# Kernel optimization log

Measured on AMD Instinct MI355X. Metric: run time of the kernel, lower is better.

## Reference

```python
import jax, jax.numpy as jnp
import numpy as np
from jax import lax

TAU = 0.1
LAMBDA_ABCD = 0.5
NUM_ANCHORS = 256
THRESH = 0.6
NEG_INF = -1e30


def sample_features(feat, anchors):
    # feat: [B,C,H,W], anchors: [B,N,2] in [0,1] (u,v). Bilinear, align_corners=False, zeros padding.
    B, C, H, W = feat.shape
    g = anchors * 2.0 - 1.0
    x = ((g[..., 0] + 1.0) * W - 1.0) / 2.0  # [B,N] pixel coords
    y = ((g[..., 1] + 1.0) * H - 1.0) / 2.0
    x0 = jnp.floor(x).astype(jnp.int32); x1 = x0 + 1
    y0 = jnp.floor(y).astype(jnp.int32); y1 = y0 + 1
    wx1 = x - x0.astype(x.dtype); wx0 = 1.0 - wx1
    wy1 = y - y0.astype(y.dtype); wy0 = 1.0 - wy1
    flat = feat.reshape(B, C, H * W)

    def gather(xi, yi):
        valid = ((xi >= 0) & (xi < W) & (yi >= 0) & (yi < H)).astype(feat.dtype)
        idx = jnp.clip(yi, 0, H - 1) * W + jnp.clip(xi, 0, W - 1)  # [B,N]
        v = jnp.take_along_axis(flat, idx[:, None, :], axis=2)  # [B,C,N]
        return v * valid[:, None, :]

    out = (gather(x0, y0) * (wx0 * wy0)[:, None, :]
           + gather(x1, y0) * (wx1 * wy0)[:, None, :]
           + gather(x0, y1) * (wx0 * wy1)[:, None, :]
           + gather(x1, y1) * (wx1 * wy1)[:, None, :])
    return out.transpose(0, 2, 1)  # [B,N,C]


def layer_norm(x, gamma, beta, eps=1e-5):
    mu = x.mean(-1, keepdims=True)
    var = ((x - mu) ** 2).mean(-1, keepdims=True)
    return (x - mu) * lax.rsqrt(var + eps) * gamma + beta


def l2norm(x, eps=1e-12):
    n = jnp.sqrt(jnp.sum(x * x, -1, keepdims=True))
    return x / jnp.maximum(n, eps)


def conv2d(x, w, b, pad):
    y = lax.conv_general_dilated(x, w, (1, 1), pad,
                                 dimension_numbers=('NCHW', 'OIHW', 'NCHW'))
    return y + b[None, :, None, None]


def setup_inputs() -> dict:
    key = jax.random.key(0)
    ks = jax.random.split(key, 12)
    B, Ct, Cs, H, W, P = 16, 1024, 512, 64, 64, 256
    s = lambda k, shp, fan: jax.random.normal(k, shp, jnp.float32) * (1.0 / np.sqrt(fan))
    return {
        'teacher_feat': jax.random.normal(ks[0], (B, Ct, H, W), jnp.float32),
        'student_feat': jax.random.normal(ks[1], (B, Cs, H, W), jnp.float32),
        'conv1_w': s(ks[2], (Ct // 2, Ct, 3, 3), Ct * 9),
        'conv1_b': jnp.zeros((Ct // 2,), jnp.float32),
        'conv2_w': s(ks[3], (1, Ct // 2, 1, 1), Ct // 2),
        'conv2_b': jnp.zeros((1,), jnp.float32),
        't_w': s(ks[4], (Ct, P), Ct), 't_b': jnp.zeros((P,), jnp.float32),
        't_g': jnp.ones((P,), jnp.float32), 't_beta': jnp.zeros((P,), jnp.float32),
        's_w': s(ks[5], (Cs, P), Cs), 's_b': jnp.zeros((P,), jnp.float32),
        's_g': jnp.ones((P,), jnp.float32), 's_beta': jnp.zeros((P,), jnp.float32),
    }


def reference(teacher_feat, student_feat, conv1_w, conv1_b, conv2_w, conv2_b,
              t_w, t_b, t_g, t_beta, s_w, s_b, s_g, s_beta):
    B, Ct, H, W = teacher_feat.shape
    # learnable anchor generator
    h = jax.nn.relu(conv2d(teacher_feat, conv1_w, conv1_b, 'SAME'))
    heatmap = jax.nn.softplus(conv2d(h, conv2_w, conv2_b, 'SAME'))  # [B,1,H,W]
    prob = heatmap.reshape(B, -1)
    prob = prob / (prob.sum(1, keepdims=True) + 1e-6)
    # multinomial without replacement via Gumbel top-k (fixed key -> deterministic)
    u01 = jax.random.uniform(jax.random.key(42), prob.shape, jnp.float32, 1e-8, 1.0)
    gumbel = -jnp.log(-jnp.log(u01))
    idx = lax.top_k(jnp.log(prob + 1e-12) + gumbel, NUM_ANCHORS)[1]  # [B,N]
    ax = (idx % W).astype(jnp.float32) / W
    ay = (idx // W).astype(jnp.float32) / H
    anchors = jnp.stack([ax, ay], -1)  # [B,N,2]

    ft = sample_features(teacher_feat, anchors)  # [B,N,Ct]
    fs = sample_features(student_feat, anchors)  # [B,N,Cs]
    ft = l2norm(layer_norm(jnp.einsum('bnc,cp->bnp', ft, t_w) + t_b, t_g, t_beta))
    fs = l2norm(layer_norm(jnp.einsum('bnc,cp->bnp', fs, s_w) + s_b, s_g, s_beta))

    loss_gafd = jnp.mean((fs - lax.stop_gradient(ft)) ** 2)

    saliency = sample_features(heatmap, anchors)[..., 0]  # [B,N]
    bd = saliency > THRESH * saliency.max(1, keepdims=True)  # [B,N] bool
    non_bd = ~bd

    pos = jnp.sum(fs * ft, -1) / TAU                       # [B,N]
    neg = jnp.einsum('bnc,bmc->bnm', fs, fs) / TAU          # [B,N,N]
    neg = jnp.where(non_bd[:, None, :], neg, NEG_INF)
    logits = jnp.concatenate([pos[..., None], neg], -1)    # [B,N,N+1]
    row_loss = jax.nn.logsumexp(logits, -1) - pos          # [B,N]

    bd_f = bd.astype(jnp.float32)
    cnt = bd_f.sum(1)
    per_b = (row_loss * bd_f).sum(1) / jnp.maximum(cnt, 1.0)
    valid = ((cnt > 0) & (non_bd.sum(1) > 0)).astype(jnp.float32)
    vnum = valid.sum()
    loss_abcd = jnp.where(vnum > 0, (per_b * valid).sum() / jnp.maximum(vnum, 1.0), 0.0)

    total_loss = loss_gafd + LAMBDA_ABCD * loss_abcd
    return total_loss, loss_gafd, loss_abcd, heatmap
```

## Files before the change

### kernel.cpp

```cpp
#include <hip/hip_runtime.h>
#include <stdint.h>


typedef float f32x4 __attribute__((ext_vector_type(4)));
typedef short s16x8 __attribute__((ext_vector_type(8)));

__device__ __forceinline__ unsigned short f2bf(float f) {
  unsigned u = __float_as_uint(f);
  u += 0x7fffu + ((u >> 16) & 1u);
  return (unsigned short)(u >> 16);
}
__device__ __forceinline__ float bf2f(unsigned short h) {
  return __uint_as_float((unsigned)h << 16);
}

__device__ __forceinline__ void gld16(const void* g, void* l) {
  __builtin_amdgcn_global_load_lds(
      (const __attribute__((address_space(1))) void*)g,
      (__attribute__((address_space(3))) void*)l, 16, 0, 0);
}

__device__ __forceinline__ float block_sum(float v, float* l4) {
  for (int m = 32; m; m >>= 1) v += __shfl_xor(v, m, 64);
  int wid = threadIdx.x >> 6;
  if ((threadIdx.x & 63) == 0) l4[wid] = v;
  __syncthreads();
  float r = l4[0] + l4[1] + l4[2] + l4[3];
  __syncthreads();
  return r;
}

__global__ void k_pad_transpose(const float* __restrict__ teacher,
                                unsigned short* __restrict__ tpad) {
  __shared__ __align__(16) unsigned short lds[64 * 65];
  int bid = blockIdx.x;
  int cb = bid & 15, y = (bid >> 4) & 63, b = bid >> 10;
  int t = threadIdx.x;
#pragma unroll
  for (int it = 0; it < 16; ++it) {
    int idx = it * 256 + t;
    int cl = idx >> 6, x = idx & 63;
    float v = teacher[(size_t)(b * 1024 + cb * 64 + cl) * 4096 + y * 64 + x];
    lds[cl * 65 + x] = f2bf(v);
  }
  __syncthreads();
  size_t obase = ((size_t)(b * 66 + y + 1) * 66 + 1) * 1024 + cb * 64;
#pragma unroll
  for (int it = 0; it < 16; ++it) {
    int x = it * 4 + (t >> 6);
    int cl = t & 63;
    tpad[obase + (size_t)x * 1024 + cl] = lds[cl * 65 + x];
  }
  if (y == 0) {
    for (int idx = t; idx < 66 * 64; idx += 256) {
      int col = idx >> 6, cl = idx & 63;
      tpad[((size_t)(b * 66) * 66 + col) * 1024 + cb * 64 + cl] = 0;
    }
  }
  if (y == 63) {
    for (int idx = t; idx < 66 * 64; idx += 256) {
      int col = idx >> 6, cl = idx & 63;
      tpad[((size_t)(b * 66 + 65) * 66 + col) * 1024 + cb * 64 + cl] = 0;
    }
  }
  if (t < 128) {
    int col = (t >= 64) ? 65 : 0;
    int cl = t & 63;
    tpad[((size_t)(b * 66 + y + 1) * 66 + col) * 1024 + cb * 64 + cl] = 0;
  }
}

__global__ void k_wprep(const float* __restrict__ w1,
                        unsigned short* __restrict__ wt) {
  __shared__ float wl[9216];
  int co = blockIdx.x, t = threadIdx.x;
  const float* src = w1 + (size_t)co * 9216;
  for (int i = t; i < 9216; i += 256) wl[i] = src[i];
  __syncthreads();
  for (int i = t; i < 9216; i += 256) {
    int tap = i >> 10;
    int ci = i - (tap << 10);
    int kb = ci >> 6, kc = ci & 63;
    wt[(size_t)tap * 524288 + (size_t)kb * 32768 + co * 64 + kc] = f2bf(wl[ci * 9 + tap]);
  }
}

__global__ void k_wT(const float* __restrict__ w, unsigned short* __restrict__ wT,
                     int K) {
  int e = blockIdx.x * 256 + threadIdx.x;
  int p = e / K, k = e - p * K;
  wT[e] = f2bf(w[(size_t)k * 256 + p]);
}

__global__ __launch_bounds__(256) void k_conv(
    const unsigned short* __restrict__ tpad, const unsigned short* __restrict__ wt,
    const float* __restrict__ b1, const float* __restrict__ w2,
    float* __restrict__ heat) {
  __shared__ __align__(16) unsigned short As[128 * 64];
  __shared__ __align__(16) unsigned short Bs[128 * 64];
  int bid = blockIdx.x;
  int nt = bid & 3, mt = bid >> 2;
  int p0 = mt * 128;
  int b = p0 >> 12, y0 = (p0 >> 6) & 63;
  int co0 = nt * 128;
  int t = threadIdx.x, wid = t >> 6, lane = t & 63;
  int wm = wid & 1, wn = wid >> 1;
  int quad = lane >> 4, l15 = lane & 15;
  int sw7 = l15 & 7;

  f32x4 acc[4][4];
  const f32x4 fz = {0.f, 0.f, 0.f, 0.f};
#pragma unroll
  for (int i = 0; i < 4; ++i)
#pragma unroll
    for (int j = 0; j < 4; ++j) acc[i][j] = fz;

  int xj[4], yrj[4];
#pragma unroll
  for (int jj = 0; jj < 4; ++jj) {
    int m = (wid * 4 + jj) * 8 + (lane >> 3);
    xj[jj] = m & 63;
    yrj[jj] = m >> 6;
  }
  int kcol = (((lane & 7) ^ ((lane >> 3) & 7))) * 8;
  int brow = ((lane >> 3) & 7) * 64;
  const unsigned short* wt_nt = wt + (size_t)co0 * 64;

  for (int tap = 0; tap < 9; ++tap) {
    int ky = tap / 3, kx = tap - ky * 3;
    size_t abase[4];
#pragma unroll
    for (int jj = 0; jj < 4; ++jj) {
      int row = y0 + yrj[jj] + ky;
      int col = xj[jj] + kx;
      abase[jj] = ((size_t)(b * 66 + row) * 66 + col) * 1024 + kcol;
    }
    size_t bbase = (size_t)tap * 16 * 32768;
    for (int kb = 0; kb < 16; ++kb) {
#pragma unroll
      for (int jj = 0; jj < 4; ++jj) {
        gld16(tpad + abase[jj] + kb * 64, (char*)As + (wid * 4 + jj) * 1024);
        gld16(wt_nt + bbase + (size_t)kb * 32768 + (wid * 4 + jj) * 512 + brow + kcol,
              (char*)Bs + (wid * 4 + jj) * 1024);
      }
      __syncthreads();
#pragma unroll
      for (int s = 0; s < 2; ++s) {
        s16x8 af[4], bf[4];
        int chunk = ((s * 4 + quad) ^ sw7) * 8;
#pragma unroll
        for (int i = 0; i < 4; ++i) {
          af[i] = *(const s16x8*)(const void*)(As + (wm * 64 + i * 16 + l15) * 64 + chunk);
          bf[i] = *(const s16x8*)(const void*)(Bs + (wn * 64 + i * 16 + l15) * 64 + chunk);
        }
#pragma unroll
        for (int i = 0; i < 4; ++i)
#pragma unroll
          for (int j = 0; j < 4; ++j)
            acc[i][j] = __builtin_amdgcn_mfma_f32_16x16x32_bf16(af[i], bf[j], acc[i][j], 0, 0, 0);
      }
      __syncthreads();
    }
  }

  float w2v[4], b1v[4];
#pragma unroll
  for (int j = 0; j < 4; ++j) {
    int co = co0 + wn * 64 + j * 16 + l15;
    w2v[j] = w2[co];
    b1v[j] = b1[co];
  }
#pragma unroll
  for (int i = 0; i < 4; ++i) {
#pragma unroll
    for (int r = 0; r < 4; ++r) {
      float part = 0.f;
#pragma unroll
      for (int j = 0; j < 4; ++j) {
        float v = acc[i][j][r] + b1v[j];
        v = fmaxf(v, 0.f);
        part += v * w2v[j];
      }
#pragma unroll
      for (int msk = 1; msk < 16; msk <<= 1) part += __shfl_xor(part, msk, 64);
      if (l15 == 0) {
        int m = wm * 64 + i * 16 + quad * 4 + r;
        atomicAdd(&heat[p0 + m], part);
      }
    }
  }
}

__device__ __forceinline__ unsigned rotl32(unsigned x, int d) {
  return (x << d) | (x >> (32 - d));
}
__device__ unsigned threefry_bits(unsigned lo) {
  const unsigned k0 = 0u, k1 = 42u;
  const unsigned k2 = 0x1BD11BDAu ^ k0 ^ k1;
  unsigned x0 = 0u + k0, x1 = lo + k1;
#define TF_R4(a, bq, c, d)                                \
  x0 += x1; x1 = rotl32(x1, a); x1 ^= x0;                 \
  x0 += x1; x1 = rotl32(x1, bq); x1 ^= x0;                \
  x0 += x1; x1 = rotl32(x1, c); x1 ^= x0;                 \
  x0 += x1; x1 = rotl32(x1, d); x1 ^= x0;
  TF_R4(13, 15, 26, 6)  x0 += k1; x1 += k2 + 1u;
  TF_R4(17, 29, 16, 24) x0 += k2; x1 += k0 + 2u;
  TF_R4(13, 15, 26, 6)  x0 += k0; x1 += k1 + 3u;
  TF_R4(17, 29, 16, 24) x0 += k1; x1 += k2 + 4u;
  TF_R4(13, 15, 26, 6)  x0 += k2; x1 += k0 + 5u;
#undef TF_R4
  return x0 ^ x1;
}

__global__ void k_heat2score(const float* __restrict__ heat, const float* __restrict__ b2p,
                             float* __restrict__ out_hm, float* __restrict__ hm,
                             float* __restrict__ scores) {
  __shared__ float l4[4];
  int b = blockIdx.x, t = threadIdx.x;
  float b2 = b2p[0];
  float hv[16];
  float lsum = 0.f;
#pragma unroll
  for (int j = 0; j < 16; ++j) {
    int e = j * 256 + t;
    float x = heat[b * 4096 + e] + b2;
    float sp = fmaxf(x, 0.f) + log1pf(expf(-fabsf(x)));
    hv[j] = sp;
    lsum += sp;
  }
  float S = block_sum(lsum, l4);
  float denom = S + 1e-6f;
#pragma unroll
  for (int j = 0; j < 16; ++j) {
    int e = j * 256 + t;
    float sp = hv[j];
    out_hm[b * 4096 + e] = sp;
    hm[b * 4096 + e] = sp;
    float lp = logf(sp / denom + 1e-12f);
    unsigned bits = threefry_bits((unsigned)(b * 4096 + e));
    float u01 = __uint_as_float((bits >> 9) | 0x3f800000u) - 1.0f;
    float u = fmaxf(1e-8f, u01 * (1.0f - 1e-8f) + 1e-8f);
    float gum = -logf(-logf(u));
    scores[b * 4096 + e] = lp + gum;
  }
}

__global__ void k_topk(const float* __restrict__ scores, int* __restrict__ idx_sel) {
  __shared__ unsigned keys[4096];
  __shared__ unsigned hist[256];
  __shared__ unsigned suf[256];
  __shared__ unsigned sel[2];
  __shared__ int wpos;
  int b = blockIdx.x, t = threadIdx.x;
#pragma unroll
  for (int j = 0; j < 16; ++j) {
    unsigned u = __float_as_uint(scores[b * 4096 + j * 256 + t]);
    u = (u >> 31) ? ~u : (u | 0x80000000u);
    keys[j * 256 + t] = u;
  }
  if (t == 0) wpos = 0;
  unsigned prefix = 0, hmask = 0, r = 256;
  for (int pass = 0; pass < 4; ++pass) {
    int shift = 24 - 8 * pass;
    hist[t] = 0;
    __syncthreads();
#pragma unroll
    for (int j = 0; j < 16; ++j) {
      unsigned u = keys[j * 256 + t];
      if ((u & hmask) == prefix) atomicAdd(&hist[(u >> shift) & 255u], 1u);
    }
    __syncthreads();
    suf[t] = hist[t];
    __syncthreads();
    for (int off = 1; off < 256; off <<= 1) {
      unsigned v = (t + off < 256) ? suf[t + off] : 0u;
      __syncthreads();
      suf[t] += v;
      __syncthreads();
    }
    unsigned above = (t < 255) ? suf[t + 1] : 0u;
    if (suf[t] >= r && above < r) {
      sel[0] = (unsigned)t;
      sel[1] = above;
    }
    __syncthreads();
    prefix |= sel[0] << shift;
    hmask |= 0xFFu << shift;
    r -= sel[1];
    __syncthreads();
  }
#pragma unroll
  for (int j = 0; j < 16; ++j) {
    int e = j * 256 + t;
    if (keys[e] > prefix) {
      int s = atomicAdd(&wpos, 1);
      idx_sel[b * 256 + s] = e;
    }
  }
  __syncthreads();
#pragma unroll
  for (int j = 0; j < 16; ++j) {
    int e = j * 256 + t;
    if (keys[e] == prefix) {
      int s = atomicAdd(&wpos, 1);
      if (s < 256) idx_sel[b * 256 + s] = e;
    }
  }
}

__global__ void k_gather_t(const unsigned short* __restrict__ tpad,
                           const int* __restrict__ idx_sel,
                           unsigned short* __restrict__ ftb) {
  int bn = blockIdx.x;
  int b = bn >> 8;
  int idx = idx_sel[bn];
  int px = idx & 63, py = idx >> 6;
  const unsigned short* base = tpad + ((size_t)(b * 66 + py) * 66 + px) * 1024;
  for (int c = threadIdx.x; c < 1024; c += 256) {
    float v = bf2f(base[c]) + bf2f(base[c + 1024]) +
              bf2f(base[c + 66 * 1024]) + bf2f(base[c + 67 * 1024]);
    ftb[(size_t)bn * 1024 + c] = f2bf(0.25f * v);
  }
}

__global__ void k_gather_s(const float* __restrict__ student,
                           const int* __restrict__ idx_sel,
                           unsigned short* __restrict__ fsbT) {
  __shared__ float plane[4096];
  int blk = blockIdx.x;
  int b = blk >> 9, c = blk & 511;
  int t = threadIdx.x;
  const float4* g4 = (const float4*)(student + ((size_t)b * 512 + c) * 4096);
  float4* p4 = (float4*)plane;
  for (int i = t; i < 1024; i += 256) p4[i] = g4[i];
  __syncthreads();
  int idx = idx_sel[b * 256 + t];
  int px = idx & 63, py = idx >> 6;
  float v = 0.f;
  if (py > 0) {
    if (px > 0) v += plane[(py - 1) * 64 + px - 1];
    v += plane[(py - 1) * 64 + px];
  }
  if (px > 0) v += plane[py * 64 + px - 1];
  v += plane[py * 64 + px];
  fsbT[((size_t)b * 512 + c) * 256 + t] = f2bf(0.25f * v);
}

__global__ void k_fsb_tr(const unsigned short* __restrict__ fsbT,
                         unsigned short* __restrict__ fsb) {
  __shared__ unsigned short tile[64][65];
  int blk = blockIdx.x;
  int b = blk >> 5, ct = (blk >> 2) & 7, nt = blk & 3;
  int t = threadIdx.x;
#pragma unroll
  for (int it = 0; it < 16; ++it) {
    int e = it * 256 + t;
    int cl = e >> 6, n = e & 63;
    tile[cl][n] = fsbT[((size_t)(b * 512 + ct * 64 + cl)) * 256 + nt * 64 + n];
  }
  __syncthreads();
#pragma unroll
  for (int it = 0; it < 16; ++it) {
    int e = it * 256 + t;
    int n = e >> 6, cl = e & 63;
    fsb[((size_t)(b * 256 + nt * 64 + n)) * 512 + ct * 64 + cl] = tile[cl][n];
  }
}

__global__ __launch_bounds__(256) void k_proj(
    const unsigned short* __restrict__ A, const unsigned short* __restrict__ Wt,
    int K, float* __restrict__ outp) {
  __shared__ __align__(16) unsigned short As[128 * 64];
  __shared__ __align__(16) unsigned short Bs[128 * 64];
  int bid = blockIdx.x;
  int nt = bid & 1, mt = bid >> 1;
  int m0 = mt * 128, n0 = nt * 128;
  int t = threadIdx.x, wid = t >> 6, lane = t & 63;
  int wm = wid & 1, wn = wid >> 1;
  int quad = lane >> 4, l15 = lane & 15;

  f32x4 acc[4][4];
  const f32x4 fz = {0.f, 0.f, 0.f, 0.f};
#pragma unroll
  for (int i = 0; i < 4; ++i)
#pragma unroll
    for (int j = 0; j < 4; ++j) acc[i][j] = fz;

  int row4[4];
#pragma unroll
  for (int jj = 0; jj < 4; ++jj) row4[jj] = (wid * 4 + jj) * 8 + (lane >> 3);
  int kcol = (lane & 7) * 8;

  int nkb = K >> 6;
  for (int kb = 0; kb < nkb; ++kb) {
#pragma unroll
    for (int jj = 0; jj < 4; ++jj) {
      gld16(A + (size_t)(m0 + row4[jj]) * K + kb * 64 + kcol,
            (char*)As + (wid * 4 + jj) * 1024);
      gld16(Wt + (size_t)(n0 + row4[jj]) * K + kb * 64 + kcol,
            (char*)Bs + (wid * 4 + jj) * 1024);
    }
    __syncthreads();
#pragma unroll
    for (int s = 0; s < 2; ++s) {
      s16x8 af[4], bf[4];
#pragma unroll
      for (int i = 0; i < 4; ++i) {
        af[i] = *(const s16x8*)(const void*)(As + (wm * 64 + i * 16 + l15) * 64 + s * 32 + quad * 8);
        bf[i] = *(const s16x8*)(const void*)(Bs + (wn * 64 + i * 16 + l15) * 64 + s * 32 + quad * 8);
      }
#pragma unroll
      for (int i = 0; i < 4; ++i)
#pragma unroll
        for (int j = 0; j < 4; ++j)
          acc[i][j] = __builtin_amdgcn_mfma_f32_16x16x32_bf16(af[i], bf[j], acc[i][j], 0, 0, 0);
    }
    __syncthreads();
  }
#pragma unroll
  for (int i = 0; i < 4; ++i)
#pragma unroll
    for (int j = 0; j < 4; ++j)
#pragma unroll
      for (int r = 0; r < 4; ++r) {
        int m = m0 + wm * 64 + i * 16 + quad * 4 + r;
        int p = n0 + wn * 64 + j * 16 + l15;
        outp[(size_t)m * 256 + p] = acc[i][j][r];
      }
}

__global__ void k_ln(const float* __restrict__ projp, const float* __restrict__ bias,
                     const float* __restrict__ g, const float* __restrict__ beta,
                     float* __restrict__ outf, unsigned short* __restrict__ outb) {
  __shared__ float l4[4];
  int row = blockIdx.x, t = threadIdx.x;
  float x = projp[(size_t)row * 256 + t] + bias[t];
  float s1 = block_sum(x, l4);
  float mu = s1 * (1.f / 256.f);
  float d = x - mu;
  float s2 = block_sum(d * d, l4);
  float rstd = rsqrtf(s2 * (1.f / 256.f) + 1e-5f);
  float xn = d * rstd * g[t] + beta[t];
  float ss = block_sum(xn * xn, l4);
  float o = xn / fmaxf(sqrtf(ss), 1e-12f);
  outf[(size_t)row * 256 + t] = o;
  if (outb) outb[(size_t)row * 256 + t] = f2bf(o);
}

__global__ void k_sal(const float* __restrict__ hm, const int* __restrict__ idx_sel,
                      int* __restrict__ bd, int* __restrict__ cnt, int* __restrict__ nbc) {
  __shared__ float l4[4];
  int b = blockIdx.x, t = threadIdx.x;
  int idx = idx_sel[b * 256 + t];
  int px = idx & 63, py = idx >> 6;
  const float* hb = hm + b * 4096;
  float v = 0.f;
  if (py > 0) {
    if (px > 0) v += hb[(py - 1) * 64 + px - 1];
    v += hb[(py - 1) * 64 + px];
  }
  if (px > 0) v += hb[py * 64 + px - 1];
  v += hb[py * 64 + px];
  float sal = 0.25f * v;
  float mx = sal;
  for (int m = 32; m; m >>= 1) mx = fmaxf(mx, __shfl_xor(mx, m, 64));
  if ((t & 63) == 0) l4[t >> 6] = mx;
  __syncthreads();
  mx = fmaxf(fmaxf(l4[0], l4[1]), fmaxf(l4[2], l4[3]));
  __syncthreads();
  int bdv = sal > 0.6f * mx ? 1 : 0;
  bd[b * 256 + t] = bdv;
  float c = block_sum((float)bdv, l4);
  if (t == 0) {
    cnt[b] = (int)c;
    nbc[b] = 256 - (int)c;
  }
}

__global__ void k_pos_gafd(const float* __restrict__ fsn, const float* __restrict__ ftn,
                           float* __restrict__ pos, float* __restrict__ gsum) {
  __shared__ float l4[4];
  int row = blockIdx.x, t = threadIdx.x;
  float a = fsn[(size_t)row * 256 + t];
  float bt = ftn[(size_t)row * 256 + t];
  float sdot = block_sum(a * bt, l4);
  if (t == 0) pos[row] = sdot * 10.f;
  float d = a - bt;
  float ssq = block_sum(d * d, l4);
  if (t == 0) atomicAdd(gsum, ssq);
}

__global__ __launch_bounds__(256) void k_abcd_rows(
    const unsigned short* __restrict__ fsnb, const int* __restrict__ bd,
    const float* __restrict__ pos, float* __restrict__ rowloss) {
  __shared__ __align__(16) unsigned short Ab[64 * 64];
  __shared__ __align__(16) unsigned short Bb[256 * 64];
  __shared__ float mrg[64][4][2];
  int b = blockIdx.x >> 2, nb = blockIdx.x & 3;
  int n0 = nb * 64;
  int t = threadIdx.x, w = t >> 6, lane = t & 63, quad = lane >> 4, l15 = lane & 15;
  f32x4 acc[4][4];
  const f32x4 fz = {0.f, 0.f, 0.f, 0.f};
#pragma unroll
  for (int i = 0; i < 4; ++i)
#pragma unroll
    for (int j = 0; j < 4; ++j) acc[i][j] = fz;
  const unsigned short* fb = fsnb + (size_t)b * 256 * 256;

  for (int kc = 0; kc < 4; ++kc) {
    {
      int r = t >> 2, cc = (t & 3) * 16;
      const uint4* s = (const uint4*)(const void*)(fb + (size_t)(n0 + r) * 256 + kc * 64 + cc);
      *(uint4*)(void*)(Ab + r * 64 + cc) = s[0];
      *(uint4*)(void*)(Ab + r * 64 + cc + 8) = s[1];
    }
#pragma unroll
    for (int it = 0; it < 4; ++it) {
      int m = it * 64 + (t >> 2), cc = (t & 3) * 16;
      const uint4* s = (const uint4*)(const void*)(fb + (size_t)m * 256 + kc * 64 + cc);
      *(uint4*)(void*)(Bb + m * 64 + cc) = s[0];
      *(uint4*)(void*)(Bb + m * 64 + cc + 8) = s[1];
    }
    __syncthreads();
#pragma unroll
    for (int s = 0; s < 2; ++s) {
      s16x8 af[4], bf[4];
#pragma unroll
      for (int i = 0; i < 4; ++i) {
        af[i] = *(const s16x8*)(const void*)(Ab + (i * 16 + l15) * 64 + s * 32 + quad * 8);
        bf[i] = *(const s16x8*)(const void*)(Bb + (w * 64 + i * 16 + l15) * 64 + s * 32 + quad * 8);
      }
#pragma unroll
      for (int i = 0; i < 4; ++i)
#pragma unroll
        for (int j = 0; j < 4; ++j)
          acc[i][j] = __builtin_amdgcn_mfma_f32_16x16x32_bf16(af[i], bf[j], acc[i][j], 0, 0, 0);
    }
    __syncthreads();
  }

  int nbmask[4];
#pragma unroll
  for (int j = 0; j < 4; ++j) nbmask[j] = bd[b * 256 + w * 64 + j * 16 + l15];
#pragma unroll
  for (int i = 0; i < 4; ++i) {
#pragma unroll
    for (int r = 0; r < 4; ++r) {
      float mxv = -1e30f, se = 0.f;
#pragma unroll
      for (int j = 0; j < 4; ++j) {
        float v = nbmask[j] ? -1e30f : (acc[i][j][r] / 0.1f);
        if (v > mxv) {
          se = se * expf(mxv - v) + 1.f;
          mxv = v;
        } else {
          se += expf(v - mxv);
        }
      }
#pragma unroll
      for (int msk = 1; msk < 16; msk <<= 1) {
        float omx = __shfl_xor(mxv, msk, 64);
        float ose = __shfl_xor(se, msk, 64);
        float nm = fmaxf(mxv, omx);
        se = se * expf(mxv - nm) + ose * expf(omx - nm);
        mxv = nm;
      }
      if (l15 == 0) {
        mrg[i * 16 + quad * 4 + r][w][0] = mxv;
        mrg[i * 16 + quad * 4 + r][w][1] = se;
      }
    }
  }
  __syncthreads();
  if (t < 64) {
    float MX = -1e30f, SE = 0.f;
    for (int ww = 0; ww < 4; ++ww) {
      float omx = mrg[t][ww][0], ose = mrg[t][ww][1];
      float nm = fmaxf(MX, omx);
      SE = SE * expf(MX - nm) + ose * expf(omx - nm);
      MX = nm;
    }
    float p = pos[b * 256 + n0 + t];
    float nm = fmaxf(MX, p);
    float se2 = SE * expf(MX - nm) + expf(p - nm);
    rowloss[b * 256 + n0 + t] = nm + logf(se2) - p;
  }
}

__global__ void k_final(const float* __restrict__ gsum, const float* __restrict__ rowloss,
                        const int* __restrict__ bd, const int* __restrict__ cnt,
                        const int* __restrict__ nbc, float* __restrict__ out) {
  __shared__ float l4[4];
  int t = threadIdx.x;
  float abcd_acc = 0.f, vnum = 0.f;
  for (int b = 0; b < 16; ++b) {
    float c = bd[b * 256 + t] ? rowloss[b * 256 + t] : 0.f;
    float s = block_sum(c, l4);
    if (t == 0) {
      float cb = (float)cnt[b];
      float per = s / fmaxf(cb, 1.f);
      if (cnt[b] > 0 && nbc[b] > 0) {
        abcd_acc += per;
        vnum += 1.f;
      }
    }
  }
  if (t == 0) {
    float gafd = gsum[0] / 1048576.f;
    float abcd = vnum > 0.f ? abcd_acc / fmaxf(vnum, 1.f) : 0.f;
    out[0] = gafd + 0.5f * abcd;
    out[1] = gafd;
    out[2] = abcd;
  }
}

static constexpr size_t OFF_TPAD = 0;
static constexpr size_t TPAD_BYTES = (size_t)16 * 66 * 66 * 1024 * 2;
static constexpr size_t OFF_WT = OFF_TPAD + TPAD_BYTES;
static constexpr size_t WT_BYTES = (size_t)9 * 16 * 512 * 64 * 2;
static constexpr size_t OFF_HEAT = OFF_WT + WT_BYTES;
static constexpr size_t OFF_GSUM = OFF_HEAT + 262144;
static constexpr size_t OFF_HM = OFF_GSUM + 256;
static constexpr size_t OFF_SC = OFF_HM + 262144;
static constexpr size_t OFF_IDX = OFF_SC + 262144;
static constexpr size_t OFF_FTB = OFF_IDX + 16384;
static constexpr size_t OFF_FSB = OFF_FTB + (size_t)4096 * 1024 * 2;
static constexpr size_t OFF_FSBT = OFF_FSB + (size_t)4096 * 512 * 2;
static constexpr size_t OFF_WTT = OFF_FSBT + (size_t)4096 * 512 * 2;
static constexpr size_t OFF_WTS = OFF_WTT + (size_t)256 * 1024 * 2;
static constexpr size_t OFF_PRT = OFF_WTS + (size_t)256 * 512 * 2;
static constexpr size_t OFF_PRS = OFF_PRT + (size_t)4096 * 256 * 4;
static constexpr size_t OFF_FTN = OFF_PRS + (size_t)4096 * 256 * 4;
static constexpr size_t OFF_FSN = OFF_FTN + (size_t)4096 * 256 * 4;
static constexpr size_t OFF_FSNB = OFF_FSN + (size_t)4096 * 256 * 4;
static constexpr size_t OFF_POS = OFF_FSNB + (size_t)4096 * 256 * 2;
static constexpr size_t OFF_BD = OFF_POS + 16384;
static constexpr size_t OFF_CNT = OFF_BD + 16384;
static constexpr size_t OFF_NBC = OFF_CNT + 64;
static constexpr size_t OFF_RL = OFF_NBC + 64;

extern "C" void kernel_launch(void* const* d_in, const int* in_sizes, int n_in,
                              void* d_out, int out_size, void* d_ws, size_t ws_size,
                              hipStream_t stream) {
  const float* teacher = (const float*)d_in[0];
  const float* student = (const float*)d_in[1];
  const float* w1 = (const float*)d_in[2];
  const float* b1 = (const float*)d_in[3];
  const float* w2 = (const float*)d_in[4];
  const float* b2 = (const float*)d_in[5];
  const float* t_w = (const float*)d_in[6];
  const float* t_b = (const float*)d_in[7];
  const float* t_g = (const float*)d_in[8];
  const float* t_be = (const float*)d_in[9];
  const float* s_w = (const float*)d_in[10];
  const float* s_b = (const float*)d_in[11];
  const float* s_g = (const float*)d_in[12];
  const float* s_be = (const float*)d_in[13];
  float* out = (float*)d_out;

  char* ws = (char*)d_ws;
  unsigned short* tpad = (unsigned short*)(ws + OFF_TPAD);
  unsigned short* wt = (unsigned short*)(ws + OFF_WT);
  float* heat = (float*)(ws + OFF_HEAT);
  float* gsum = (float*)(ws + OFF_GSUM);
  float* hm = (float*)(ws + OFF_HM);
  float* scores = (float*)(ws + OFF_SC);
  int* idx_sel = (int*)(ws + OFF_IDX);
  unsigned short* ftb = (unsigned short*)(ws + OFF_FTB);
  unsigned short* fsb = (unsigned short*)(ws + OFF_FSB);
  unsigned short* fsbT = (unsigned short*)(ws + OFF_FSBT);
  unsigned short* wTt = (unsigned short*)(ws + OFF_WTT);
  unsigned short* wTs = (unsigned short*)(ws + OFF_WTS);
  float* projt = (float*)(ws + OFF_PRT);
  float* projs = (float*)(ws + OFF_PRS);
  float* ftn = (float*)(ws + OFF_FTN);
  float* fsn = (float*)(ws + OFF_FSN);
  unsigned short* fsnb = (unsigned short*)(ws + OFF_FSNB);
  float* pos = (float*)(ws + OFF_POS);
  int* bd = (int*)(ws + OFF_BD);
  int* cnt = (int*)(ws + OFF_CNT);
  int* nbc = (int*)(ws + OFF_NBC);
  float* rowloss = (float*)(ws + OFF_RL);

  hipMemsetAsync(ws + OFF_HEAT, 0, 262144 + 256, stream);

  k_pad_transpose<<<16384, 256, 0, stream>>>(teacher, tpad);
  k_wprep<<<512, 256, 0, stream>>>(w1, wt);
  k_wT<<<1024, 256, 0, stream>>>(t_w, wTt, 1024);
  k_wT<<<512, 256, 0, stream>>>(s_w, wTs, 512);
  k_conv<<<2048, 256, 0, stream>>>(tpad, wt, b1, w2, heat);
  k_heat2score<<<16, 256, 0, stream>>>(heat, b2, out + 3, hm, scores);
  k_topk<<<16, 256, 0, stream>>>(scores, idx_sel);
  k_gather_t<<<4096, 256, 0, stream>>>(tpad, idx_sel, ftb);
  k_gather_s<<<8192, 256, 0, stream>>>(student, idx_sel, fsbT);
  k_fsb_tr<<<512, 256, 0, stream>>>(fsbT, fsb);
  k_proj<<<64, 256, 0, stream>>>(ftb, wTt, 1024, projt);
  k_proj<<<64, 256, 0, stream>>>(fsb, wTs, 512, projs);
  k_ln<<<4096, 256, 0, stream>>>(projt, t_b, t_g, t_be, ftn, (unsigned short*)nullptr);
  k_ln<<<4096, 256, 0, stream>>>(projs, s_b, s_g, s_be, fsn, fsnb);
  k_sal<<<16, 256, 0, stream>>>(hm, idx_sel, bd, cnt, nbc);
  k_pos_gafd<<<4096, 256, 0, stream>>>(fsn, ftn, pos, gsum);
  k_abcd_rows<<<64, 256, 0, stream>>>(fsnb, bd, pos, rowloss);
  k_final<<<1, 256, 0, stream>>>(gsum, rowloss, bd, cnt, nbc, out);
}
```

Before: 1.346 ms.

## Rewrite conv GEMM with 256x256 tiles, double-buffered LDS and phased MFMA scheduling

The implicit-GEMM 3x3 conv kernel moves from 128x128 tiles with 256 threads and one LDS buffer to 256x256 tiles with 512 threads and double-buffered LDS. Global-to-LDS loads for the next k-step are interleaved with MFMA phases, using explicit barriers, waitcnts and setprio. A block-id swizzle groups blocks for L2 reuse. The larger tiles cut global traffic per FLOP, at the cost of more registers and LDS per block (launch_bounds 512,2) and fragile hand-written synchronisation.

```diff
diff --git a/kernel.cpp b/kernel.cpp
--- a/kernel.cpp
+++ b/kernel.cpp
@@ -92,86 +92,165 @@
   wT[e] = f2bf(w[(size_t)k * 256 + p]);
 }
 
-__global__ __launch_bounds__(256) void k_conv(
+#define STAGE_A(buf, ts, h) do {                                              \
+    int tap_ = (ts) >> 4, kb_ = (ts) & 15;                                    \
+    int ky_ = tap_ / 3, kx_ = tap_ - ky_ * 3;                                 \
+    unsigned o_ = (unsigned)(((ky_ * 66 + kx_) << 10) + (kb_ << 6));          \
+    gld16(tpad + aoff[(h) * 2 + 0] + o_,                                      \
+          (char*)(As[buf] + (((h) * 128 + wid * 8) << 6)));                   \
+    gld16(tpad + aoff[(h) * 2 + 1] + o_,                                      \
+          (char*)(As[buf] + (((h) * 128 + 64 + wid * 8) << 6)));              \
+  } while (0)
+
+#define STAGE_B(buf, ts, h) do {                                              \
+    int tap_ = (ts) >> 4, kb_ = (ts) & 15;                                    \
+    unsigned o_ = (unsigned)((tap_ << 19) + (kb_ << 15));                     \
+    gld16(wt + boff[(h) * 2 + 0] + o_,                                        \
+          (char*)(Bs[buf] + (((h) * 128 + wid * 8) << 6)));                   \
+    gld16(wt + boff[(h) * 2 + 1] + o_,                                        \
+          (char*)(Bs[buf] + (((h) * 128 + 64 + wid * 8) << 6)));              \
+  } while (0)
+
+#define LDA8(AF, buf, i0)                                                     \
+  _Pragma("unroll") for (int i_ = 0; i_ < 4; ++i_)                            \
+  _Pragma("unroll") for (int s_ = 0; s_ < 2; ++s_)                            \
+    AF[i_][s_] = *(const s16x8*)(const void*)(                                \
+        &As[buf][(wm * 128 + ((i0) + i_) * 16 + l15) * 64 +                   \
+                 ((s_ * 4 + quad) ^ sw7) * 8]);
+
+#define LDB4(BF, buf, j0)                                                     \
+  _Pragma("unroll") for (int j_ = 0; j_ < 2; ++j_)                            \
+  _Pragma("unroll") for (int s_ = 0; s_ < 2; ++s_)                            \
+    BF[j_][s_] = *(const s16x8*)(const void*)(                                \
+        &Bs[buf][(wn * 64 + ((j0) + j_) * 16 + l15) * 64 +                    \
+                 ((s_ * 4 + quad) ^ sw7) * 8]);
+
+#define MFMA16(AF, BF, i0, j0)                                                \
+  _Pragma("unroll") for (int i_ = 0; i_ < 4; ++i_)                            \
+  _Pragma("unroll") for (int j_ = 0; j_ < 2; ++j_)                            \
+  _Pragma("unroll") for (int s_ = 0; s_ < 2; ++s_)                            \
+    acc[(i0) + i_][(j0) + j_] = __builtin_amdgcn_mfma_f32_16x16x32_bf16(      \
+        AF[i_][s_], BF[j_][s_], acc[(i0) + i_][(j0) + j_], 0, 0, 0);
+
+#define PHASE_MID()                                                           \
+  __builtin_amdgcn_s_barrier();                                               \
+  asm volatile("s_waitcnt lgkmcnt(0)" ::: "memory");                          \
+  __builtin_amdgcn_sched_barrier(0);                                          \
+  __builtin_amdgcn_s_setprio(1)
+
+#define PHASE_END()                                                           \
+  __builtin_amdgcn_s_setprio(0);                                              \
+  __builtin_amdgcn_sched_barrier(0);                                          \
+  __builtin_amdgcn_s_barrier()
+
+#define PHASE_END_VM()                                                        \
+  __builtin_amdgcn_s_setprio(0);                                              \
+  __builtin_amdgcn_sched_barrier(0);                                          \
+  asm volatile("s_waitcnt vmcnt(4)" ::: "memory");                            \
+  __builtin_amdgcn_s_barrier()
+
+__global__ __launch_bounds__(512, 2) void k_conv(
     const unsigned short* __restrict__ tpad, const unsigned short* __restrict__ wt,
     const float* __restrict__ b1, const float* __restrict__ w2,
     float* __restrict__ heat) {
-  __shared__ __align__(16) unsigned short As[128 * 64];
-  __shared__ __align__(16) unsigned short Bs[128 * 64];
+  __shared__ __align__(16) unsigned short As[2][256 * 64];
+  __shared__ __align__(16) unsigned short Bs[2][256 * 64];
   int bid = blockIdx.x;
-  int nt = bid & 3, mt = bid >> 2;
-  int p0 = mt * 128;
-  int b = p0 >> 12, y0 = (p0 >> 6) & 63;
-  int co0 = nt * 128;
+  int swz = (bid & 7) * 64 + (bid >> 3);
+  int nt = swz & 1, mt = swz >> 1;
+  int m0 = mt * 256, n0 = nt * 256;
   int t = threadIdx.x, wid = t >> 6, lane = t & 63;
-  int wm = wid & 1, wn = wid >> 1;
+  int wm = wid >> 2, wn = wid & 3;
   int quad = lane >> 4, l15 = lane & 15;
   int sw7 = l15 & 7;
 
-  f32x4 acc[4][4];
+  int srcChunk = (t & 7) ^ ((t >> 3) & 7);
+  unsigned aoff[4], boff[4];
+#pragma unroll
+  for (int v = 0; v < 4; ++v) {
+    int row = (v >> 1) * 128 + (v & 1) * 64 + (t >> 3);
+    int m = m0 + row;
+    int b = m >> 12, y = (m >> 6) & 63, x = m & 63;
+    aoff[v] = (unsigned)((((b * 66 + y) * 66 + x) << 10) + srcChunk * 8);
+    boff[v] = (unsigned)(((n0 + row) << 6) + srcChunk * 8);
+  }
+
+  f32x4 acc[8][4];
   const f32x4 fz = {0.f, 0.f, 0.f, 0.f};
 #pragma unroll
-  for (int i = 0; i < 4; ++i)
+  for (int i = 0; i < 8; ++i)
 #pragma unroll
     for (int j = 0; j < 4; ++j) acc[i][j] = fz;
 
-  int xj[4], yrj[4];
-#pragma unroll
-  for (int jj = 0; jj < 4; ++jj) {
-    int m = (wid * 4 + jj) * 8 + (lane >> 3);
-    xj[jj] = m & 63;
-    yrj[jj] = m >> 6;
-  }
-  int kcol = (((lane & 7) ^ ((lane >> 3) & 7))) * 8;
-  int brow = ((lane >> 3) & 7) * 64;
-  const unsigned short* wt_nt = wt + (size_t)co0 * 64;
-
-  for (int tap = 0; tap < 9; ++tap) {
-    int ky = tap / 3, kx = tap - ky * 3;
-    size_t abase[4];
-#pragma unroll
-    for (int jj = 0; jj < 4; ++jj) {
-      int row = y0 + yrj[jj] + ky;
-      int col = xj[jj] + kx;
-      abase[jj] = ((size_t)(b * 66 + row) * 66 + col) * 1024 + kcol;
-    }
-    size_t bbase = (size_t)tap * 16 * 32768;
-    for (int kb = 0; kb < 16; ++kb) {
-#pragma unroll
-      for (int jj = 0; jj < 4; ++jj) {
-        gld16(tpad + abase[jj] + kb * 64, (char*)As + (wid * 4 + jj) * 1024);
-        gld16(wt_nt + bbase + (size_t)kb * 32768 + (wid * 4 + jj) * 512 + brow + kcol,
-              (char*)Bs + (wid * 4 + jj) * 1024);
-      }
-      __syncthreads();
-#pragma unroll
-      for (int s = 0; s < 2; ++s) {
-        s16x8 af[4], bf[4];
-        int chunk = ((s * 4 + quad) ^ sw7) * 8;
-#pragma unroll
-        for (int i = 0; i < 4; ++i) {
-          af[i] = *(const s16x8*)(const void*)(As + (wm * 64 + i * 16 + l15) * 64 + chunk);
-          bf[i] = *(const s16x8*)(const void*)(Bs + (wn * 64 + i * 16 + l15) * 64 + chunk);
-        }
-#pragma unroll
-        for (int i = 0; i < 4; ++i)
-#pragma unroll
-          for (int j = 0; j < 4; ++j)
-            acc[i][j] = __builtin_amdgcn_mfma_f32_16x16x32_bf16(af[i], bf[j], acc[i][j], 0, 0, 0);
-      }
-      __syncthreads();
-    }
+  STAGE_B(0, 0, 0); STAGE_B(0, 0, 1);
+  STAGE_A(0, 0, 0); STAGE_A(0, 0, 1);
+  STAGE_B(1, 1, 0); STAGE_B(1, 1, 1);
+  asm volatile("s_waitcnt vmcnt(4)" ::: "memory");
+  __builtin_amdgcn_s_barrier();
+
+  for (int it2 = 0; it2 < 72; ++it2) {
+    int T0 = it2 * 2, T1 = T0 + 1;
+    int tsN0 = (T0 + 2 <= 143) ? T0 + 2 : 143;
+    int tsN1 = (T1 + 2 <= 143) ? T1 + 2 : 143;
+    s16x8 af[4][2], bf01[2][2], bf23[2][2];
+    LDA8(af, 0, 0);
+    LDB4(bf01, 0, 0);
+    STAGE_A(1, T1, 0);
+    PHASE_MID();
+    MFMA16(af, bf01, 0, 0);
+    PHASE_END();
+
+    LDB4(bf23, 0, 2);
+    STAGE_A(1, T1, 1);
+    PHASE_MID();
+    MFMA16(af, bf23, 0, 2);
+    PHASE_END();
+
+    LDA8(af, 0, 4);
+    STAGE_B(0, tsN0, 0);
+    PHASE_MID();
+    MFMA16(af, bf01, 4, 0);
+    PHASE_END();
+
+    STAGE_B(0, tsN0, 1);
+    PHASE_MID();
+    MFMA16(af, bf23, 4, 2);
+    PHASE_END_VM();
+
+    LDA8(af, 1, 0);
+    LDB4(bf01, 1, 0);
+    STAGE_A(0, tsN0, 0);
+    PHASE_MID();
+    MFMA16(af, bf01, 0, 0);
+    PHASE_END();
+
+    LDB4(bf23, 1, 2);
+    STAGE_A(0, tsN0, 1);
+    PHASE_MID();
+    MFMA16(af, bf23, 0, 2);
+    PHASE_END();
+
+    LDA8(af, 1, 4);
+    STAGE_B(1, tsN1, 0);
+    PHASE_MID();
+    MFMA16(af, bf01, 4, 0);
+    PHASE_END();
+
+    STAGE_B(1, tsN1, 1);
+    PHASE_MID();
+    MFMA16(af, bf23, 4, 2);
+    PHASE_END_VM();
   }
 
   float w2v[4], b1v[4];
 #pragma unroll
   for (int j = 0; j < 4; ++j) {
-    int co = co0 + wn * 64 + j * 16 + l15;
+    int co = n0 + wn * 64 + j * 16 + l15;
     w2v[j] = w2[co];
     b1v[j] = b1[co];
   }
 #pragma unroll
-  for (int i = 0; i < 4; ++i) {
+  for (int i = 0; i < 8; ++i) {
 #pragma unroll
     for (int r = 0; r < 4; ++r) {
       float part = 0.f;
@@ -183,10 +262,7 @@
       }
 #pragma unroll
       for (int msk = 1; msk < 16; msk <<= 1) part += __shfl_xor(part, msk, 64);
-      if (l15 == 0) {
-        int m = wm * 64 + i * 16 + quad * 4 + r;
-        atomicAdd(&heat[p0 + m], part);
-      }
+      if (l15 == 0) atomicAdd(&heat[m0 + wm * 128 + i * 16 + quad * 4 + r], part);
     }
   }
 }
@@ -688,7 +764,7 @@
   k_wprep<<<512, 256, 0, stream>>>(w1, wt);
   k_wT<<<1024, 256, 0, stream>>>(t_w, wTt, 1024);
   k_wT<<<512, 256, 0, stream>>>(s_w, wTs, 512);
-  k_conv<<<2048, 256, 0, stream>>>(tpad, wt, b1, w2, heat);
+  k_conv<<<512, 512, 0, stream>>>(tpad, wt, b1, w2, heat);
   k_heat2score<<<16, 256, 0, stream>>>(heat, b2, out + 3, hm, scores);
   k_topk<<<16, 256, 0, stream>>>(scores, idx_sel);
   k_gather_t<<<4096, 256, 0, stream>>>(tpad, idx_sel, ftb);
```

Measured after the change: 1.194 ms. 1.13x faster.
